# Performance work log

Hardware: AMD Instinct MI355X
Metric: run time of the kernel (lower is better)

## Reference

```python
import jax, jax.numpy as jnp
import numpy as np

N, D, E = 100000, 32, 1600000
EH, NH = 32, 16
TAU = 0.1


def setup_inputs() -> dict:
    key = jax.random.key(0)
    ks = jax.random.split(key, 12)
    x = jax.random.normal(ks[0], (N, D), dtype=jnp.float32)
    edge_index = jax.random.randint(ks[1], (2, E), 0, N, dtype=jnp.int32)
    hsd = jax.random.normal(ks[2], (N,), dtype=jnp.float32)
    s_e1 = 1.0 / np.sqrt(D + 2)
    s_e2 = 1.0 / np.sqrt(EH)
    s_n2 = 1.0 / np.sqrt(NH)
    We1 = jax.random.uniform(ks[3], (D + 2, EH), jnp.float32, -s_e1, s_e1)
    be1 = jax.random.uniform(ks[4], (EH,), jnp.float32, -s_e1, s_e1)
    We2 = jax.random.uniform(ks[5], (EH, 1), jnp.float32, -s_e2, s_e2)
    be2 = jax.random.uniform(ks[6], (1,), jnp.float32, -s_e2, s_e2)
    Wn1 = jax.random.uniform(ks[7], (1, NH), jnp.float32, -1.0, 1.0)
    bn1 = jax.random.uniform(ks[8], (NH,), jnp.float32, -1.0, 1.0)
    Wn2 = jax.random.uniform(ks[9], (NH, 1), jnp.float32, -s_n2, s_n2)
    bn2 = jax.random.uniform(ks[10], (1,), jnp.float32, -s_n2, s_n2)
    return {"x": x, "hsd": hsd, "We1": We1, "be1": be1, "We2": We2, "be2": be2,
            "Wn1": Wn1, "bn1": bn1, "Wn2": Wn2, "bn2": bn2, "edge_index": edge_index}


def reference(x, hsd, We1, be1, We2, be2, Wn1, bn1, Wn2, bn2, edge_index):
    row, col = edge_index[0], edge_index[1]
    n = x.shape[0]
    # normalized HSD (torch.std is unbiased, ddof=1)
    hsd_norm = (hsd - hsd.mean()) / (jnp.std(hsd, ddof=1) + 1e-8)
    # edge MLP input: [hsd_u, hsd_v, |x_u - x_v|]  -> (E, D+2)
    diff_abs = jnp.abs(x[row] - x[col])
    edge_in = jnp.concatenate([hsd_norm[row][:, None], hsd_norm[col][:, None], diff_abs], axis=1)
    h = jax.nn.relu(edge_in @ We1 + be1)
    e_uv = (h @ We2 + be2)[:, 0]  # (E,)
    # segment softmax over destination (col)
    logits = e_uv / TAU
    seg_max = jax.ops.segment_max(logits, col, num_segments=n)
    seg_max = jnp.where(jnp.isfinite(seg_max), seg_max, 0.0)
    ex = jnp.exp(logits - seg_max[col])
    denom = jax.ops.segment_sum(ex, col, num_segments=n)
    alpha_uv = (ex / (denom[col] + 1e-16))[:, None]  # (E,1)
    # node-level gate
    gh = jax.nn.relu(hsd_norm[:, None] @ Wn1 + bn1)
    alpha_bar = jax.nn.sigmoid(gh @ Wn2 + bn2)  # (N,1)
    # degree normalization
    ones = jnp.ones(row.shape[0], dtype=x.dtype)
    src_deg = jnp.sqrt(jnp.clip(jax.ops.segment_sum(ones, row, num_segments=n), 1.0))
    dst_deg = jnp.sqrt(jnp.clip(jax.ops.segment_sum(ones, col, num_segments=n), 1.0))
    edge_w = 1.0 / (src_deg[row] * dst_deg[col])
    low_pass = jax.ops.segment_sum(edge_w[:, None] * x[row], col, num_segments=n)
    high_pass = jax.ops.segment_sum(alpha_uv * (x[col] - x[row]), col, num_segments=n)
    return (1.0 - alpha_bar) * low_pass + alpha_bar * high_pass
```

## Files before the change

kernel.cpp:

```cpp
#include <hip/hip_runtime.h>

#define D_FEAT 32
#define IN_DIM 34
#define EHID 32
#define NHID 16
#define INV_TAU 10.0f
#define SCAN_CHUNK 1024
#define EPB 256
#define XS 36
#define TILE 8192
#define CAP 6144

__global__ __launch_bounds__(256) void k1_hsd_stats(const float* __restrict__ hsd,
                                                    double* __restrict__ stats, int N) {
    double s = 0.0, s2 = 0.0;
    for (int i = blockIdx.x * 256 + threadIdx.x; i < N; i += gridDim.x * 256) {
        double v = (double)hsd[i];
        s += v; s2 += v * v;
    }
    for (int off = 32; off > 0; off >>= 1) {
        s  += __shfl_down(s,  off, 64);
        s2 += __shfl_down(s2, off, 64);
    }
    __shared__ double ls[4], ls2[4];
    int wid = threadIdx.x >> 6, lid = threadIdx.x & 63;
    if (lid == 0) { ls[wid] = s; ls2[wid] = s2; }
    __syncthreads();
    if (threadIdx.x == 0) {
        double ts = 0.0, t2 = 0.0;
        for (int w = 0; w < 4; ++w) { ts += ls[w]; t2 += ls2[w]; }
        atomicAdd(stats, ts);
        atomicAdd(stats + 1, t2);
    }
}

__global__ __launch_bounds__(256) void k2_node_prep(const float* __restrict__ hsd,
                                                    const double* __restrict__ stats,
                                                    const float* __restrict__ Wn1,
                                                    const float* __restrict__ bn1,
                                                    const float* __restrict__ Wn2,
                                                    const float* __restrict__ bn2,
                                                    float* __restrict__ hsd_norm,
                                                    float* __restrict__ alpha_bar, int N) {
    int n = blockIdx.x * 256 + threadIdx.x;
    if (n >= N) return;
    double sum = stats[0], sumsq = stats[1];
    double mean = sum / (double)N;
    double var  = (sumsq - sum * sum / (double)N) / (double)(N - 1);
    float stdv  = (float)sqrt(var);
    float hn = (hsd[n] - (float)mean) / (stdv + 1e-8f);
    hsd_norm[n] = hn;
    float acc = bn2[0];
#pragma unroll
    for (int k = 0; k < NHID; ++k)
        acc += fmaxf(fmaf(hn, Wn1[k], bn1[k]), 0.0f) * Wn2[k];
    alpha_bar[n] = 1.0f / (1.0f + __expf(-acc));
}

__global__ __launch_bounds__(256) void s1_hist(const int* __restrict__ ei,
                                               int* __restrict__ hist,
                                               int E, int NB, int T, int M) {
    __shared__ int hv[512], hu[512];
    int t = threadIdx.x;
    for (int b = t; b < 512; b += 256) { hv[b] = 0; hu[b] = 0; }
    __syncthreads();
    int base = blockIdx.x * TILE;
    for (int i = t; i < TILE; i += 256) {
        int e = base + i;
        if (e < E) {
            int u = ei[e], v = ei[E + e];
            atomicAdd(&hv[v >> 8], 1);
            atomicAdd(&hu[u >> 8], 1);
        }
    }
    __syncthreads();
    for (int b = t; b < NB; b += 256) {
        hist[b * T + blockIdx.x] = hv[b];
        hist[M + b * T + blockIdx.x] = hu[b];
    }
}

__global__ __launch_bounds__(256) void scan_k1(const int* __restrict__ cnt,
                                               int* __restrict__ out,
                                               int* __restrict__ partials, int N) {
    __shared__ int lds[256];
    int base = blockIdx.x * SCAN_CHUNK;
    int t = threadIdx.x;
    int v[4]; int loc = 0;
#pragma unroll
    for (int k = 0; k < 4; ++k) {
        int idx = base + t * 4 + k;
        v[k] = (idx < N) ? cnt[idx] : 0;
        loc += v[k];
    }
    lds[t] = loc; __syncthreads();
    for (int off = 1; off < 256; off <<= 1) {
        int a = (t >= off) ? lds[t - off] : 0;
        __syncthreads();
        lds[t] += a;
        __syncthreads();
    }
    int run = (t > 0) ? lds[t - 1] : 0;
    if (t == 255) partials[blockIdx.x] = lds[255];
#pragma unroll
    for (int k = 0; k < 4; ++k) {
        run += v[k];
        int idx = base + t * 4 + k;
        if (idx < N) out[idx + 1] = run;
    }
    if (blockIdx.x == 0 && t == 0) out[0] = 0;
}

__global__ __launch_bounds__(256) void scan_k2(int* __restrict__ partials, int B) {
    __shared__ int lds[256];
    int t = threadIdx.x;
    lds[t] = (t < B) ? partials[t] : 0;
    __syncthreads();
    for (int off = 1; off < 256; off <<= 1) {
        int a = (t >= off) ? lds[t - off] : 0;
        __syncthreads();
        lds[t] += a;
        __syncthreads();
    }
    if (t < B) partials[t] = (t > 0) ? lds[t - 1] : 0;
}

__global__ __launch_bounds__(256) void scan_k3(int* __restrict__ out,
                                               const int* __restrict__ partials, int N) {
    int i = blockIdx.x * 256 + threadIdx.x;
    if (i >= N) return;
    out[i + 1] += partials[i / SCAN_CHUNK];
}

__global__ __launch_bounds__(256) void s2_scatter(const int* __restrict__ ei,
                                                  const int* __restrict__ scanAll,
                                                  int2* __restrict__ coarse,
                                                  int* __restrict__ coarseU,
                                                  int E, int NB, int T, int M) {
    __shared__ int curV[512], curU[512];
    int t = threadIdx.x;
    for (int b = t; b < NB; b += 256) {
        curV[b] = scanAll[b * T + blockIdx.x];
        curU[b] = scanAll[M + b * T + blockIdx.x] - E;
    }
    __syncthreads();
    int base = blockIdx.x * TILE;
    for (int i = t; i < TILE; i += 256) {
        int e = base + i;
        if (e < E) {
            int u = ei[e], v = ei[E + e];
            int pv = atomicAdd(&curV[v >> 8], 1);
            coarse[pv] = make_int2(u, v);
            int pu = atomicAdd(&curU[u >> 8], 1);
            coarseU[pu] = u;
        }
    }
}

__global__ __launch_bounds__(256) void s3b_srccnt(const int* __restrict__ coarseU,
                                                  const int* __restrict__ scanAll,
                                                  int* __restrict__ src_cnt,
                                                  int N, int E, int NB, int T, int M) {
    __shared__ int cnt[256];
    int t = threadIdx.x;
    int bin = blockIdx.x;
    int start = scanAll[M + bin * T] - E;
    int endv  = scanAll[M + (bin + 1) * T] - E;
    cnt[t] = 0;
    __syncthreads();
    for (int i = start + t; i < endv; i += 256) atomicAdd(&cnt[coarseU[i] & 255], 1);
    __syncthreads();
    int vglob = (bin << 8) + t;
    if (vglob < N) src_cnt[vglob] = cnt[t];
}

__global__ __launch_bounds__(256) void k3c_mlp(const float* __restrict__ x,
                                               const float* __restrict__ hsd_norm,
                                               const float* __restrict__ We1,
                                               const float* __restrict__ be1,
                                               const float* __restrict__ We2,
                                               const float* __restrict__ be2,
                                               const int2* __restrict__ esorted,
                                               float* __restrict__ logit, int E) {
    __shared__ float sxu[EPB * XS];
    int t = threadIdx.x;
    int base = blockIdx.x * EPB;

    int q = t & 7;
#pragma unroll
    for (int k = 0; k < 8; ++k) {
        int s = (t >> 3) + 32 * k;
        int e = base + s;
        int u = esorted[(e < E) ? e : (E - 1)].x;
        float4 val = *(const float4*)(x + (size_t)u * D_FEAT + 4 * q);
        *(float4*)(sxu + s * XS + 4 * q) = val;
    }
    __syncthreads();

    int e = base + t;
    if (e >= E) return;
    int2 uv = esorted[e];
    int u = uv.x, v = uv.y;

    float in0 = hsd_norm[u];
    float in1 = hsd_norm[v];

    float diff[D_FEAT];
    const float4* xv = (const float4*)(x + (size_t)v * D_FEAT);
#pragma unroll
    for (int qq = 0; qq < 8; ++qq) {
        float4 a = *(const float4*)(sxu + t * XS + 4 * qq);
        float4 b = xv[qq];
        diff[4 * qq + 0] = fabsf(a.x - b.x);
        diff[4 * qq + 1] = fabsf(a.y - b.y);
        diff[4 * qq + 2] = fabsf(a.z - b.z);
        diff[4 * qq + 3] = fabsf(a.w - b.w);
    }

    float h[EHID];
#pragma unroll
    for (int j = 0; j < EHID; ++j)
        h[j] = fmaf(in0, We1[j], fmaf(in1, We1[EHID + j], be1[j]));
#pragma unroll
    for (int i = 0; i < D_FEAT; ++i) {
        float a = diff[i];
#pragma unroll
        for (int j = 0; j < EHID; ++j)
            h[j] = fmaf(a, We1[(i + 2) * EHID + j], h[j]);
    }
    float acc = be2[0];
#pragma unroll
    for (int j = 0; j < EHID; ++j)
        acc += fmaxf(h[j], 0.0f) * We2[j];

    logit[e] = acc * INV_TAU;
}

__global__ __launch_bounds__(512) void k6_bin(const float* __restrict__ x,
                                              const int2* __restrict__ coarse,
                                              const float* __restrict__ logit,
                                              const int* __restrict__ scanAll,
                                              const int* __restrict__ src_cnt,
                                              const float* __restrict__ alpha_bar,
                                              float* __restrict__ out,
                                              int N, int E, int NB, int T) {
    __shared__ int   u_pk[CAP];
    __shared__ float lg[CAP];
    __shared__ unsigned short sidx[CAP];
    __shared__ int cnt[256], base[256], cur[256];

    int t = threadIdx.x;
    int bin = blockIdx.x;
    int start = scanAll[bin * T];
    int n = scanAll[(bin + 1) * T] - start;
    if (n > CAP) n = CAP;

    if (t < 256) cnt[t] = 0;
    __syncthreads();
    for (int i = t; i < n; i += 512) {
        int2 c = coarse[start + i];
        int vl = c.y & 255;
        u_pk[i] = c.x | (vl << 17);
        lg[i] = logit[start + i];
        atomicAdd(&cnt[vl], 1);
    }
    __syncthreads();
    for (int off = 1; off < 256; off <<= 1) {
        int a = 0;
        if (t < 256 && t >= off) a = cnt[t - off];
        __syncthreads();
        if (t < 256) cnt[t] += a;
        __syncthreads();
    }
    if (t < 256) { base[t] = (t > 0) ? cnt[t - 1] : 0; cur[t] = base[t]; }
    __syncthreads();
    for (int i = t; i < n; i += 512) {
        int vl = u_pk[i] >> 17;
        int p = atomicAdd(&cur[vl], 1);
        sidx[p] = (unsigned short)i;
    }
    __syncthreads();

    int w = t >> 6, lane = t & 63, h = lane >> 5, l = lane & 31;
    int proc = w * 2 + h;
    for (int k = proc; k < 256; k += 16) {
        int vg = (bin << 8) + k;
        if (vg >= N) continue;
        int beg = base[k], end = cnt[k];
        int deg = end - beg;
        float* orow = out + (size_t)vg * D_FEAT;
        if (deg == 0) { orow[l] = 0.0f; continue; }

        float m = -INFINITY;
        for (int i = beg + l; i < end; i += 32) m = fmaxf(m, lg[sidx[i]]);
#pragma unroll
        for (int off = 1; off < 32; off <<= 1) m = fmaxf(m, __shfl_xor(m, off, 32));
        float s = 0.0f;
        for (int i = beg + l; i < end; i += 32) s += __expf(lg[sidx[i]] - m);
#pragma unroll
        for (int off = 1; off < 32; off <<= 1) s += __shfl_xor(s, off, 32);
        float inv_den = 1.0f / (s + 1e-16f);

        float ab = alpha_bar[vg];
        float one_ab = 1.0f - ab;
        float inv_sdv = rsqrtf((float)deg);

        float acc = 0.0f;
        int i = beg;
        for (; i + 1 < end; i += 2) {
            int e0 = sidx[i], e1 = sidx[i + 1];
            int up0 = u_pk[e0], up1 = u_pk[e1];
            int u0 = up0 & 0x1FFFF, u1 = up1 & 0x1FFFF;
            float lg0 = lg[e0], lg1 = lg[e1];
            float x0 = x[(size_t)u0 * D_FEAT + l];
            float x1 = x[(size_t)u1 * D_FEAT + l];
            float is0 = rsqrtf(fmaxf((float)src_cnt[u0], 1.0f));
            float is1 = rsqrtf(fmaxf((float)src_cnt[u1], 1.0f));
            float c0 = fmaf(-ab * __expf(lg0 - m), inv_den, one_ab * is0 * inv_sdv);
            float c1 = fmaf(-ab * __expf(lg1 - m), inv_den, one_ab * is1 * inv_sdv);
            acc = fmaf(c0, x0, acc);
            acc = fmaf(c1, x1, acc);
        }
        if (i < end) {
            int e0 = sidx[i];
            int u0 = u_pk[e0] & 0x1FFFF;
            float x0 = x[(size_t)u0 * D_FEAT + l];
            float is0 = rsqrtf(fmaxf((float)src_cnt[u0], 1.0f));
            float c0 = fmaf(-ab * __expf(lg[e0] - m), inv_den, one_ab * is0 * inv_sdv);
            acc = fmaf(c0, x0, acc);
        }
        float S = s * inv_den;
        orow[l] = fmaf(ab * S, x[(size_t)vg * D_FEAT + l], acc);
    }
}

extern "C" void kernel_launch(void* const* d_in, const int* in_sizes, int n_in,
                              void* d_out, int out_size, void* d_ws, size_t ws_size,
                              hipStream_t stream) {
    const float* x    = (const float*)d_in[0];
    const float* hsd  = (const float*)d_in[1];
    const float* We1  = (const float*)d_in[2];
    const float* be1  = (const float*)d_in[3];
    const float* We2  = (const float*)d_in[4];
    const float* be2  = (const float*)d_in[5];
    const float* Wn1  = (const float*)d_in[6];
    const float* bn1  = (const float*)d_in[7];
    const float* Wn2  = (const float*)d_in[8];
    const float* bn2  = (const float*)d_in[9];
    const int*   ei   = (const int*)d_in[10];
    float* out = (float*)d_out;

    const int N = in_sizes[1];
    const int E = in_sizes[10] / 2;
    const int NB = (N + 255) >> 8;
    const int T  = (E + TILE - 1) / TILE;
    const int M  = NB * T;
    const int M2 = 2 * M;

    char* ws = (char*)d_ws;
    size_t o = 0;
    auto alloc = [&](size_t bytes) { size_t r = o; o += (bytes + 255) & ~(size_t)255; return r; };
    double* stats     = (double*)(ws + alloc(16));
    int*    src_cnt   = (int*)(ws + alloc((size_t)4 * N));
    float*  hsd_norm  = (float*)(ws + alloc((size_t)4 * N));
    float*  alpha_bar = (float*)(ws + alloc((size_t)4 * N));
    int*    partials  = (int*)(ws + alloc(1024));
    int*    bufH      = (int*)(ws + alloc((size_t)4 * M2));
    int*    bufS      = (int*)(ws + alloc((size_t)4 * (M2 + 1)));
    int2*   coarse    = (int2*)(ws + alloc((size_t)8 * E));
    int*    coarseU   = (int*)(ws + alloc((size_t)4 * E));
    float*  logit     = (float*)coarseU;

    hipMemsetAsync(d_ws, 0, 256, stream);

    k1_hsd_stats<<<256, 256, 0, stream>>>(hsd, stats, N);
    k2_node_prep<<<(N + 255) / 256, 256, 0, stream>>>(hsd, stats, Wn1, bn1, Wn2, bn2,
                                                      hsd_norm, alpha_bar, N);

    s1_hist<<<T, 256, 0, stream>>>(ei, bufH, E, NB, T, M);

    int Bs = (M2 + SCAN_CHUNK - 1) / SCAN_CHUNK;
    scan_k1<<<Bs, 256, 0, stream>>>(bufH, bufS, partials, M2);
    scan_k2<<<1, 256, 0, stream>>>(partials, Bs);
    scan_k3<<<(M2 + 255) / 256, 256, 0, stream>>>(bufS, partials, M2);

    s2_scatter<<<T, 256, 0, stream>>>(ei, bufS, coarse, coarseU, E, NB, T, M);
    s3b_srccnt<<<NB, 256, 0, stream>>>(coarseU, bufS, src_cnt, N, E, NB, T, M);
    k3c_mlp<<<(E + EPB - 1) / EPB, 256, 0, stream>>>(x, hsd_norm, We1, be1, We2, be2,
                                                     coarse, logit, E);
    k6_bin<<<NB, 512, 0, stream>>>(x, coarse, logit, bufS, src_cnt, alpha_bar,
                                   out, N, E, NB, T);
}
```

Measured before the change: 315.8 us.

## Split binned softmax/aggregation into coefficient table and per-node gather kernels

The fused per-bin kernel, which computed softmax stats and gathered x rows with only 391 blocks, is split in two. A table kernel computes the segment max with atomicMax on order-preserving encoded floats and the denominators with shared atomics. It then writes a per-edge combined coefficient and source index into a CSR layout. A separate gather kernel with one wave per destination node does the weighted x-row accumulation at much higher parallelism, and the inverse sqrt source degree is now precomputed once per node. This costs extra global writes and reads of 2 arrays of E entries and one more launch, and CSR order within a node is now nondeterministic.

Result: no change. 314.5 us (-0.4%).

```diff
diff --git a/kernel.cpp b/kernel.cpp
--- a/kernel.cpp
+++ b/kernel.cpp
@@ -10,6 +10,15 @@
 #define XS 36
 #define TILE 8192
 #define CAP 6144
+
+__device__ __forceinline__ unsigned enc_f32(float f) {
+    unsigned b = __float_as_uint(f);
+    return (b & 0x80000000u) ? ~b : (b | 0x80000000u);
+}
+__device__ __forceinline__ float dec_f32(unsigned e) {
+    unsigned b = (e & 0x80000000u) ? (e & 0x7fffffffu) : ~e;
+    return __uint_as_float(b);
+}
 
 __global__ __launch_bounds__(256) void k1_hsd_stats(const float* __restrict__ hsd,
                                                     double* __restrict__ stats, int N) {
@@ -159,7 +168,7 @@
 
 __global__ __launch_bounds__(256) void s3b_srccnt(const int* __restrict__ coarseU,
                                                   const int* __restrict__ scanAll,
-                                                  int* __restrict__ src_cnt,
+                                                  float* __restrict__ inv_ssrc,
                                                   int N, int E, int NB, int T, int M) {
     __shared__ int cnt[256];
     int t = threadIdx.x;
@@ -171,7 +180,7 @@
     for (int i = start + t; i < endv; i += 256) atomicAdd(&cnt[coarseU[i] & 255], 1);
     __syncthreads();
     int vglob = (bin << 8) + t;
-    if (vglob < N) src_cnt[vglob] = cnt[t];
+    if (vglob < N) inv_ssrc[vglob] = rsqrtf(fmaxf((float)cnt[t], 1.0f));
 }
 
 __global__ __launch_bounds__(256) void k3c_mlp(const float* __restrict__ x,
@@ -236,18 +245,22 @@
     logit[e] = acc * INV_TAU;
 }
 
-__global__ __launch_bounds__(512) void k6_bin(const float* __restrict__ x,
-                                              const int2* __restrict__ coarse,
-                                              const float* __restrict__ logit,
-                                              const int* __restrict__ scanAll,
-                                              const int* __restrict__ src_cnt,
-                                              const float* __restrict__ alpha_bar,
-                                              float* __restrict__ out,
-                                              int N, int E, int NB, int T) {
-    __shared__ int   u_pk[CAP];
-    __shared__ float lg[CAP];
-    __shared__ unsigned short sidx[CAP];
-    __shared__ int cnt[256], base[256], cur[256];
+__global__ __launch_bounds__(512) void k6a_tab(const int2* __restrict__ coarse,
+                                               const float* __restrict__ logit,
+                                               const int* __restrict__ scanAll,
+                                               const float* __restrict__ inv_ssrc,
+                                               const float* __restrict__ alpha_bar,
+                                               int* __restrict__ usrc,
+                                               float* __restrict__ coefG,
+                                               int* __restrict__ dst_off,
+                                               float* __restrict__ selfc,
+                                               int N, int E, int NB, int T) {
+    __shared__ int      su[CAP];
+    __shared__ float    slg[CAP];
+    __shared__ int      cnt[256];
+    __shared__ unsigned mEnc[256];
+    __shared__ float    den[256], cA[256], cB[256];
+    __shared__ int      base_[256], cur_[256];
 
     int t = threadIdx.x;
     int bin = blockIdx.x;
@@ -255,16 +268,26 @@
     int n = scanAll[(bin + 1) * T] - start;
     if (n > CAP) n = CAP;
 
-    if (t < 256) cnt[t] = 0;
-    __syncthreads();
+    if (t < 256) { cnt[t] = 0; mEnc[t] = 0u; den[t] = 0.0f; }
+    __syncthreads();
+
     for (int i = t; i < n; i += 512) {
         int2 c = coarse[start + i];
+        float lgv = logit[start + i];
         int vl = c.y & 255;
-        u_pk[i] = c.x | (vl << 17);
-        lg[i] = logit[start + i];
+        su[i] = c.x | (vl << 17);
+        slg[i] = lgv;
         atomicAdd(&cnt[vl], 1);
-    }
-    __syncthreads();
+        atomicMax(&mEnc[vl], enc_f32(lgv));
+    }
+    __syncthreads();
+
+    for (int i = t; i < n; i += 512) {
+        int vl = su[i] >> 17;
+        atomicAdd(&den[vl], __expf(slg[i] - dec_f32(mEnc[vl])));
+    }
+    __syncthreads();
+
     for (int off = 1; off < 256; off <<= 1) {
         int a = 0;
         if (t < 256 && t >= off) a = cnt[t - off];
@@ -272,66 +295,71 @@
         if (t < 256) cnt[t] += a;
         __syncthreads();
     }
-    if (t < 256) { base[t] = (t > 0) ? cnt[t - 1] : 0; cur[t] = base[t]; }
-    __syncthreads();
+    if (t < 256) {
+        int b0 = (t > 0) ? cnt[t - 1] : 0;
+        base_[t] = b0; cur_[t] = b0;
+        int vg = (bin << 8) + t;
+        if (vg < N) {
+            float ab = alpha_bar[vg];
+            float d = den[t];
+            float inv_den = 1.0f / (d + 1e-16f);
+            int deg = cnt[t] - b0;
+            cA[t] = -ab * inv_den;
+            cB[t] = (1.0f - ab) * rsqrtf(fmaxf((float)deg, 1.0f));
+            dst_off[vg] = start + b0;
+            selfc[vg] = ab * (d * inv_den);
+        }
+    }
+    if (bin == 0 && t == 0) dst_off[N] = E;
+    __syncthreads();
+
     for (int i = t; i < n; i += 512) {
-        int vl = u_pk[i] >> 17;
-        int p = atomicAdd(&cur[vl], 1);
-        sidx[p] = (unsigned short)i;
-    }
-    __syncthreads();
-
-    int w = t >> 6, lane = t & 63, h = lane >> 5, l = lane & 31;
-    int proc = w * 2 + h;
-    for (int k = proc; k < 256; k += 16) {
-        int vg = (bin << 8) + k;
-        if (vg >= N) continue;
-        int beg = base[k], end = cnt[k];
-        int deg = end - beg;
-        float* orow = out + (size_t)vg * D_FEAT;
-        if (deg == 0) { orow[l] = 0.0f; continue; }
-
-        float m = -INFINITY;
-        for (int i = beg + l; i < end; i += 32) m = fmaxf(m, lg[sidx[i]]);
-#pragma unroll
-        for (int off = 1; off < 32; off <<= 1) m = fmaxf(m, __shfl_xor(m, off, 32));
-        float s = 0.0f;
-        for (int i = beg + l; i < end; i += 32) s += __expf(lg[sidx[i]] - m);
-#pragma unroll
-        for (int off = 1; off < 32; off <<= 1) s += __shfl_xor(s, off, 32);
-        float inv_den = 1.0f / (s + 1e-16f);
-
-        float ab = alpha_bar[vg];
-        float one_ab = 1.0f - ab;
-        float inv_sdv = rsqrtf((float)deg);
-
-        float acc = 0.0f;
-        int i = beg;
-        for (; i + 1 < end; i += 2) {
-            int e0 = sidx[i], e1 = sidx[i + 1];
-            int up0 = u_pk[e0], up1 = u_pk[e1];
-            int u0 = up0 & 0x1FFFF, u1 = up1 & 0x1FFFF;
-            float lg0 = lg[e0], lg1 = lg[e1];
-            float x0 = x[(size_t)u0 * D_FEAT + l];
-            float x1 = x[(size_t)u1 * D_FEAT + l];
-            float is0 = rsqrtf(fmaxf((float)src_cnt[u0], 1.0f));
-            float is1 = rsqrtf(fmaxf((float)src_cnt[u1], 1.0f));
-            float c0 = fmaf(-ab * __expf(lg0 - m), inv_den, one_ab * is0 * inv_sdv);
-            float c1 = fmaf(-ab * __expf(lg1 - m), inv_den, one_ab * is1 * inv_sdv);
-            acc = fmaf(c0, x0, acc);
-            acc = fmaf(c1, x1, acc);
-        }
-        if (i < end) {
-            int e0 = sidx[i];
-            int u0 = u_pk[e0] & 0x1FFFF;
-            float x0 = x[(size_t)u0 * D_FEAT + l];
-            float is0 = rsqrtf(fmaxf((float)src_cnt[u0], 1.0f));
-            float c0 = fmaf(-ab * __expf(lg[e0] - m), inv_den, one_ab * is0 * inv_sdv);
-            acc = fmaf(c0, x0, acc);
-        }
-        float S = s * inv_den;
-        orow[l] = fmaf(ab * S, x[(size_t)vg * D_FEAT + l], acc);
-    }
+        int up = su[i];
+        int vl = up >> 17;
+        int u = up & 0x1FFFF;
+        int p = start + atomicAdd(&cur_[vl], 1);
+        float coef = fmaf(cA[vl], __expf(slg[i] - dec_f32(mEnc[vl])), cB[vl] * inv_ssrc[u]);
+        usrc[p] = u;
+        coefG[p] = coef;
+    }
+}
+
+__global__ __launch_bounds__(256) void k7_gather(const float* __restrict__ x,
+                                                 const int* __restrict__ dst_off,
+                                                 const int* __restrict__ usrc,
+                                                 const float* __restrict__ coefG,
+                                                 const float* __restrict__ selfc,
+                                                 float* __restrict__ out, int N) {
+    int wid = threadIdx.x >> 6;
+    int lane = threadIdx.x & 63;
+    int v = blockIdx.x * 4 + wid;
+    if (v >= N) return;
+
+    int beg = dst_off[v], end = dst_off[v + 1];
+    int half = lane >> 5;
+    int l = lane & 31;
+
+    float acc = 0.0f;
+    int jj = beg + half;
+    for (; jj + 2 < end; jj += 4) {
+        int u0 = usrc[jj];
+        int u1 = usrc[jj + 2];
+        float c0 = coefG[jj];
+        float c1 = coefG[jj + 2];
+        float x0 = x[(size_t)u0 * D_FEAT + l];
+        float x1 = x[(size_t)u1 * D_FEAT + l];
+        acc = fmaf(c0, x0, acc);
+        acc = fmaf(c1, x1, acc);
+    }
+    for (; jj < end; jj += 2) {
+        int u0 = usrc[jj];
+        float c0 = coefG[jj];
+        acc = fmaf(c0, x[(size_t)u0 * D_FEAT + l], acc);
+    }
+    acc += __shfl_xor(acc, 32, 64);
+
+    if (half == 0)
+        out[(size_t)v * D_FEAT + l] = fmaf(selfc[v], x[(size_t)v * D_FEAT + l], acc);
 }
 
 extern "C" void kernel_launch(void* const* d_in, const int* in_sizes, int n_in,
@@ -361,15 +389,19 @@
     size_t o = 0;
     auto alloc = [&](size_t bytes) { size_t r = o; o += (bytes + 255) & ~(size_t)255; return r; };
     double* stats     = (double*)(ws + alloc(16));
-    int*    src_cnt   = (int*)(ws + alloc((size_t)4 * N));
+    float*  inv_ssrc  = (float*)(ws + alloc((size_t)4 * N));
     float*  hsd_norm  = (float*)(ws + alloc((size_t)4 * N));
     float*  alpha_bar = (float*)(ws + alloc((size_t)4 * N));
+    float*  selfc     = (float*)(ws + alloc((size_t)4 * N));
+    int*    dst_off   = (int*)(ws + alloc((size_t)4 * (N + 1)));
     int*    partials  = (int*)(ws + alloc(1024));
     int*    bufH      = (int*)(ws + alloc((size_t)4 * M2));
     int*    bufS      = (int*)(ws + alloc((size_t)4 * (M2 + 1)));
     int2*   coarse    = (int2*)(ws + alloc((size_t)8 * E));
     int*    coarseU   = (int*)(ws + alloc((size_t)4 * E));
     float*  logit     = (float*)coarseU;
+    int*    usrc      = (int*)(ws + alloc((size_t)4 * E));
+    float*  coefG     = (float*)(ws + alloc((size_t)4 * E));
 
     hipMemsetAsync(d_ws, 0, 256, stream);
 
@@ -385,9 +417,10 @@
     scan_k3<<<(M2 + 255) / 256, 256, 0, stream>>>(bufS, partials, M2);
 
     s2_scatter<<<T, 256, 0, stream>>>(ei, bufS, coarse, coarseU, E, NB, T, M);
-    s3b_srccnt<<<NB, 256, 0, stream>>>(coarseU, bufS, src_cnt, N, E, NB, T, M);
+    s3b_srccnt<<<NB, 256, 0, stream>>>(coarseU, bufS, inv_ssrc, N, E, NB, T, M);
     k3c_mlp<<<(E + EPB - 1) / EPB, 256, 0, stream>>>(x, hsd_norm, We1, be1, We2, be2,
                                                      coarse, logit, E);
-    k6_bin<<<NB, 512, 0, stream>>>(x, coarse, logit, bufS, src_cnt, alpha_bar,
-                                   out, N, E, NB, T);
-}
+    k6a_tab<<<NB, 512, 0, stream>>>(coarse, logit, bufS, inv_ssrc, alpha_bar,
+                                    usrc, coefG, dst_off, selfc, N, E, NB, T);
+    k7_gather<<<(N + 3) / 4, 256, 0, stream>>>(x, dst_off, usrc, coefG, selfc, out, N);
+}
```
